# Kernel optimization log

Hardware: AMD Instinct MI355X
Metric: run time of the kernel (lower is better)

The kernel has to match this reference:

```python
import jax, jax.numpy as jnp
from jax import lax
import numpy as np

B, D, K = 4096, 128, 8192          # batch, embedding_dim, num_embeddings
LATENT_C, LATENT_H, LATENT_W = 64, 7, 7
OUT_H, OUT_W = 84, 84              # observation_shape H, W (decoder resizes 56->84)


def setup_inputs() -> dict:
    key = jax.random.key(0)
    ks = jax.random.split(key, 10)
    z = jax.random.normal(ks[0], (B, D), dtype=jnp.float32)
    # codebook init: uniform(-1/K, 1/K) as in torch module
    codebook = jax.random.uniform(ks[1], (K, D), jnp.float32, -1.0 / K, 1.0 / K)
    lin_w = jax.random.normal(ks[2], (LATENT_C * LATENT_H * LATENT_W, D), jnp.float32) * 0.02
    lin_b = jnp.zeros((LATENT_C * LATENT_H * LATENT_W,), jnp.float32)
    # ConvTranspose2d weights in torch layout (in_ch, out_ch, kH, kW)
    w1 = jax.random.normal(ks[3], (64, 64, 4, 4), jnp.float32) * 0.02
    b1 = jnp.zeros((64,), jnp.float32)
    w2 = jax.random.normal(ks[4], (64, 32, 4, 4), jnp.float32) * 0.02
    b2 = jnp.zeros((32,), jnp.float32)
    w3 = jax.random.normal(ks[5], (32, 1, 4, 4), jnp.float32) * 0.02
    b3 = jnp.zeros((1,), jnp.float32)
    return {"z": z, "codebook": codebook, "lin_w": lin_w, "lin_b": lin_b,
            "w1": w1, "b1": b1, "w2": w2, "b2": b2, "w3": w3, "b3": b3}


def _conv_transpose(x, w, b):
    """PyTorch ConvTranspose2d(k=4, stride=2, pad=1) via lhs-dilated conv.
    w is torch layout (in, out, kH, kW); flip spatially and swap in/out -> OIHW."""
    wk = jnp.flip(w, axis=(2, 3)).transpose(1, 0, 2, 3)  # (out, in, kH, kW)
    y = lax.conv_general_dilated(
        x, wk, window_strides=(1, 1), padding=((2, 2), (2, 2)),
        lhs_dilation=(2, 2), dimension_numbers=("NCHW", "OIHW", "NCHW"))
    return y + b[None, :, None, None]


def reference(z, codebook, lin_w, lin_b, w1, b1, w2, b2, w3, b3):
    # --- VectorQuantizer ---
    # squared L2 distances: ||z||^2 + ||e||^2 - 2 z e^T  -> (B, K)
    d2 = (jnp.sum(z * z, axis=1, keepdims=True)
          + jnp.sum(codebook * codebook, axis=1)
          - 2.0 * (z @ codebook.T))
    indices = jnp.argmin(d2, axis=1)              # (B,)
    z_q = codebook[indices]                       # gather (B, D)
    codebook_loss = jnp.mean((lax.stop_gradient(z) - z_q) ** 2)
    commitment_loss = jnp.mean((z - lax.stop_gradient(z_q)) ** 2)
    z_q_st = z + lax.stop_gradient(z_q - z)       # straight-through
    # --- VQVAEDecoder ---
    x = z_q_st @ lin_w.T + lin_b                  # (B, 64*7*7)
    x = x.reshape(-1, LATENT_C, LATENT_H, LATENT_W)
    x = jax.nn.relu(_conv_transpose(x, w1, b1))   # (B, 64, 14, 14)
    x = jax.nn.relu(_conv_transpose(x, w2, b2))   # (B, 32, 28, 28)
    x = _conv_transpose(x, w3, b3)                # (B, 1, 56, 56)
    # bilinear resize, align_corners=False (half-pixel centers)
    x = jax.image.resize(x, (x.shape[0], 1, OUT_H, OUT_W), method="bilinear")
    recon = jnp.tanh(x)
    return recon, indices, codebook_loss, commitment_loss
```

## Files before the change

### kernel.cpp

```cpp
#include <hip/hip_runtime.h>
#include <math.h>

#define B_SZ    4096
#define D_DIM   128
#define K_CODES 8192
#define RECON_N (4096*84*84)

__global__ __attribute__((amdgpu_flat_work_group_size(1024,1024),
                          amdgpu_waves_per_eu(4,8)))
void vq_kernel(
    const float* __restrict__ z, const float* __restrict__ cb,
    int* __restrict__ idx_ws, float* __restrict__ out_idx_f,
    double* __restrict__ lpart)
{
  __shared__ float z_s[16][128];
  __shared__ float zz_s[16];
  __shared__ float redv[16][16];
  __shared__ int   redi[16][16];
  __shared__ int   win[16];
  __shared__ double wsum[16];
  const int t  = threadIdx.x;
  const int b0 = blockIdx.x * 16;

  for (int p = t; p < 2048; p += 1024) z_s[p >> 7][p & 127] = z[(size_t)b0*128 + p];
  __syncthreads();

  if (t < 16) {
    #pragma clang fp contract(off)
    const float* a = z_s[t];
    float r8[8];
    #pragma unroll
    for (int j = 0; j < 8; j++) { float v = a[j]*a[j]; r8[j] = v; }
    for (int i = 8; i < 128; i += 8) {
      #pragma unroll
      for (int j = 0; j < 8; j++) { float v = a[i+j]*a[i+j]; r8[j] = r8[j] + v; }
    }
    zz_s[t] = ((r8[0]+r8[1]) + (r8[2]+r8[3])) + ((r8[4]+r8[5]) + (r8[6]+r8[7]));
  }
  __syncthreads();

  const int lane = t & 63, wv = t >> 6;
  float zzr[16];
  #pragma unroll
  for (int row = 0; row < 16; row++) zzr[row] = zz_s[row];

  float best[16]; int bid[16];
  #pragma unroll
  for (int row = 0; row < 16; row++) { best[row] = INFINITY; bid[row] = 0; }

  #pragma unroll 1
  for (int k = 0; k < 8; k++) {
    const int cg   = wv + (k << 4);
    const int code = (cg << 6) + lane;
    const float* ep = cb + (size_t)code * 128;
    float r[16];
    #pragma unroll
    for (int row = 0; row < 16; row++) r[row] = 0.0f;
    #pragma unroll 1
    for (int d16 = 0; d16 < 8; d16++) {
      const float4 e0 = *(const float4*)(ep + d16*16 + 0);
      const float4 e1 = *(const float4*)(ep + d16*16 + 4);
      const float4 e2 = *(const float4*)(ep + d16*16 + 8);
      const float4 e3 = *(const float4*)(ep + d16*16 + 12);
      #pragma unroll
      for (int row = 0; row < 16; row++) {
        const float4 z0 = *(const float4*)(&z_s[row][d16*16 + 0]);
        const float4 z1 = *(const float4*)(&z_s[row][d16*16 + 4]);
        const float4 z2 = *(const float4*)(&z_s[row][d16*16 + 8]);
        const float4 z3 = *(const float4*)(&z_s[row][d16*16 + 12]);
        float rr = r[row];
        rr = fmaf(z0.x,e0.x,rr); rr = fmaf(z0.y,e0.y,rr); rr = fmaf(z0.z,e0.z,rr); rr = fmaf(z0.w,e0.w,rr);
        rr = fmaf(z1.x,e1.x,rr); rr = fmaf(z1.y,e1.y,rr); rr = fmaf(z1.z,e1.z,rr); rr = fmaf(z1.w,e1.w,rr);
        rr = fmaf(z2.x,e2.x,rr); rr = fmaf(z2.y,e2.y,rr); rr = fmaf(z2.z,e2.z,rr); rr = fmaf(z2.w,e2.w,rr);
        rr = fmaf(z3.x,e3.x,rr); rr = fmaf(z3.y,e3.y,rr); rr = fmaf(z3.z,e3.z,rr); rr = fmaf(z3.w,e3.w,rr);
        r[row] = rr;
      }
    }
    #pragma unroll
    for (int row = 0; row < 16; row++) {
      const float tt = fmaf(-2.0f, r[row], zzr[row]);
      if (tt < best[row]) { best[row] = tt; bid[row] = code; }
    }
  }

  #pragma unroll 1
  for (int row = 0; row < 16; row++) {
    float v = best[row]; int i = bid[row];
    #pragma unroll
    for (int m = 32; m; m >>= 1) {
      float v2 = __shfl_xor(v, m, 64);
      int   i2 = __shfl_xor(i, m, 64);
      if (v2 < v || (v2 == v && i2 < i)) { v = v2; i = i2; }
    }
    if (lane == 0) { redv[wv][row] = v; redi[wv][row] = i; }
  }
  __syncthreads();

  if (t < 16) {
    float v = redv[0][t]; int i = redi[0][t];
    #pragma unroll 1
    for (int w = 1; w < 16; w++) {
      float v2 = redv[w][t]; int i2 = redi[w][t];
      if (v2 < v || (v2 == v && i2 < i)) { v = v2; i = i2; }
    }
    win[t] = i;
    idx_ws[b0 + t] = i;
    out_idx_f[b0 + t] = (float)i;
  }
  __syncthreads();

  double ls = 0.0;
  for (int p = t; p < 2048; p += 1024) {
    int r = p >> 7, d = p & 127;
    float diff = z_s[r][d] - cb[(size_t)win[r]*128 + d];
    ls = fma((double)diff, (double)diff, ls);
  }
  #pragma unroll
  for (int m = 32; m; m >>= 1) ls += __shfl_xor(ls, m, 64);
  if (lane == 0) wsum[wv] = ls;
  __syncthreads();
  if (t == 0) {
    double s = 0.0;
    for (int w = 0; w < 16; w++) s += wsum[w];
    lpart[blockIdx.x] = s;
  }
}

__global__ __launch_bounds__(256) void fin_kernel(const double* __restrict__ lpart,
                                                  float* __restrict__ out_loss)
{
  __shared__ double s[256];
  const int t = threadIdx.x;
  s[t] = lpart[t];
  __syncthreads();
  for (int off = 128; off; off >>= 1) {
    if (t < off) s[t] += s[t + off];
    __syncthreads();
  }
  if (t == 0) {
    float l = (float)(s[0] / (4096.0*128.0));
    out_loss[0] = l;
    out_loss[1] = l;
  }
}

__global__ __launch_bounds__(256) void linear_kernel(
    const float* __restrict__ cb, const int* __restrict__ idx,
    const float* __restrict__ lw, const float* __restrict__ lb,
    float* __restrict__ x1)
{
  __shared__ float As[64][65];
  __shared__ float Bs[64][65];
  __shared__ int idx_s[64];
  const int t  = threadIdx.x;
  const int b0 = blockIdx.x * 64, n0 = blockIdx.y * 64;
  if (t < 64) idx_s[t] = idx[b0 + t];
  float acc[4][4] = {{0.f}};
  const int tr = (t >> 4)*4, tc = (t & 15)*4;
  for (int d0 = 0; d0 < 128; d0 += 64) {
    __syncthreads();
    #pragma unroll
    for (int l = 0; l < 16; l++) {
      int flat = t + l*256;
      int r = flat >> 6, d = flat & 63;
      As[r][d] = cb[(size_t)idx_s[r]*128 + d0 + d];
      Bs[r][d] = lw[(size_t)(n0 + r)*128 + d0 + d];
    }
    __syncthreads();
    #pragma unroll 8
    for (int d = 0; d < 64; d++) {
      float a0 = As[tr+0][d], a1 = As[tr+1][d], a2 = As[tr+2][d], a3 = As[tr+3][d];
      float q0 = Bs[tc+0][d], q1 = Bs[tc+1][d], q2 = Bs[tc+2][d], q3 = Bs[tc+3][d];
      acc[0][0] = fmaf(a0,q0,acc[0][0]); acc[0][1] = fmaf(a0,q1,acc[0][1]);
      acc[0][2] = fmaf(a0,q2,acc[0][2]); acc[0][3] = fmaf(a0,q3,acc[0][3]);
      acc[1][0] = fmaf(a1,q0,acc[1][0]); acc[1][1] = fmaf(a1,q1,acc[1][1]);
      acc[1][2] = fmaf(a1,q2,acc[1][2]); acc[1][3] = fmaf(a1,q3,acc[1][3]);
      acc[2][0] = fmaf(a2,q0,acc[2][0]); acc[2][1] = fmaf(a2,q1,acc[2][1]);
      acc[2][2] = fmaf(a2,q2,acc[2][2]); acc[2][3] = fmaf(a2,q3,acc[2][3]);
      acc[3][0] = fmaf(a3,q0,acc[3][0]); acc[3][1] = fmaf(a3,q1,acc[3][1]);
      acc[3][2] = fmaf(a3,q2,acc[3][2]); acc[3][3] = fmaf(a3,q3,acc[3][3]);
    }
  }
  #pragma unroll
  for (int i = 0; i < 4; i++)
    #pragma unroll
    for (int j = 0; j < 4; j++)
      x1[(size_t)(b0 + tr + i)*3136 + n0 + tc + j] = acc[i][j] + lb[n0 + tc + j];
}

#define DA_T 896
#define B1_CS 260
#define IMG_FL (64*B1_CS)
__global__ __attribute__((amdgpu_flat_work_group_size(DA_T, DA_T),
                          amdgpu_waves_per_eu(4, 4)))
void decoder_a(
    const float* __restrict__ x1,
    const float* __restrict__ w1, const float* __restrict__ b1,
    const float* __restrict__ w2, const float* __restrict__ b2,
    float* __restrict__ a2, int b_off, int n_img)
{
  extern __shared__ float B1s[];
  const int tid = threadIdx.x;
  const int b   = blockIdx.x;
  const int iA  = 2*b;
  const bool hasB = (iA + 1) < n_img;
  const int gA  = b_off + iA;

  for (int p = tid; p < 2*IMG_FL; p += DA_T) B1s[p] = 0.0f;
  __syncthreads();

  {
    const int c = tid & 63, y = tid >> 6;
    const int ky0 = (y & 1) ? 0 : 1;
    const int iy0 = (y + 1 - ky0) >> 1;
    const int iy1 = iy0 - 1;
    const bool v0 = (iy0 < 7), v1 = (iy1 >= 0);
    const float bias = b1[c];
    float accA[14], accB[14];
    #pragma unroll
    for (int x = 0; x < 14; x++) { accA[x] = bias; accB[x] = bias; }
    const float* ximA = x1 + (size_t)gA*3136;
    const float* ximB = hasB ? (ximA + 3136) : ximA;
    #pragma unroll 1
    for (int i = 0; i < 64; i++) {
      const float* wp = w1 + (((i << 6) + c) << 4) + ky0*4;
      const float4 wA4 = *(const float4*)(wp);
      const float4 wB4 = *(const float4*)(wp + 8);
      const float wa[4] = {wA4.x, wA4.y, wA4.z, wA4.w};
      const float wb[4] = {wB4.x, wB4.y, wB4.z, wB4.w};
      float r0A[7], r1A[7], r0B[7], r1B[7];
      if (v0) {
        const float* xr = ximA + i*49 + iy0*7;
        const float* xs = ximB + i*49 + iy0*7;
        #pragma unroll
        for (int j = 0; j < 7; j++) { r0A[j] = xr[j]; r0B[j] = xs[j]; }
      } else {
        #pragma unroll
        for (int j = 0; j < 7; j++) { r0A[j] = 0.0f; r0B[j] = 0.0f; }
      }
      if (v1) {
        const float* xr = ximA + i*49 + iy1*7;
        const float* xs = ximB + i*49 + iy1*7;
        #pragma unroll
        for (int j = 0; j < 7; j++) { r1A[j] = xr[j]; r1B[j] = xs[j]; }
      } else {
        #pragma unroll
        for (int j = 0; j < 7; j++) { r1A[j] = 0.0f; r1B[j] = 0.0f; }
      }
      #pragma unroll
      for (int x = 0; x < 14; x++) {
        const int kxs = (x & 1) ? 0 : 1;
        const int ix0 = (x + 1 - kxs) >> 1;
        const int ix1 = ix0 - 1;
        float s = accA[x];
        if (ix0 < 7)  { s = fmaf(r0A[ix0], wa[kxs],   s); s = fmaf(r1A[ix0], wb[kxs],   s); }
        if (ix1 >= 0) { s = fmaf(r0A[ix1], wa[kxs+2], s); s = fmaf(r1A[ix1], wb[kxs+2], s); }
        accA[x] = s;
      }
      #pragma unroll
      for (int x = 0; x < 14; x++) {
        const int kxs = (x & 1) ? 0 : 1;
        const int ix0 = (x + 1 - kxs) >> 1;
        const int ix1 = ix0 - 1;
        float s = accB[x];
        if (ix0 < 7)  { s = fmaf(r0B[ix0], wa[kxs],   s); s = fmaf(r1B[ix0], wb[kxs],   s); }
        if (ix1 >= 0) { s = fmaf(r0B[ix1], wa[kxs+2], s); s = fmaf(r1B[ix1], wb[kxs+2], s); }
        accB[x] = s;
      }
    }
    float* oA = &B1s[c*B1_CS + (y + 1)*16 + 1];
    float* oB = oA + IMG_FL;
    #pragma unroll
    for (int x = 0; x < 14; x++) oA[x] = fmaxf(accA[x], 0.0f);
    #pragma unroll
    for (int x = 0; x < 14; x++) oB[x] = fmaxf(accB[x], 0.0f);
  }
  __syncthreads();

  {
    const int c = tid & 31, y = tid >> 5;
    const int ky0 = (y & 1) ? 0 : 1;
    const int iy0 = (y + 1 - ky0) >> 1;
    const int row0 = iy0 + 1;
    const int row1 = iy0;
    const float bias = b2[c];
    const int nimg = hasB ? 2 : 1;
    #pragma unroll 1
    for (int img = 0; img < nimg; img++) {
      const float* base = &B1s[img*IMG_FL];
      float acc[28];
      #pragma unroll
      for (int x = 0; x < 28; x++) acc[x] = bias;
      #pragma unroll 1
      for (int i = 0; i < 64; i++) {
        const float* wp = w2 + (((i << 5) + c) << 4) + ky0*4;
        const float4 wA4 = *(const float4*)(wp);
        const float4 wB4 = *(const float4*)(wp + 8);
        const float wa[4] = {wA4.x, wA4.y, wA4.z, wA4.w};
        const float wb[4] = {wB4.x, wB4.y, wB4.z, wB4.w};
        const float* rp0 = base + i*B1_CS + row0*16;
        const float* rp1 = base + i*B1_CS + row1*16;
        float r0[16], r1[16];
        #pragma unroll
        for (int q = 0; q < 4; q++) {
          const float4 a4 = *(const float4*)(rp0 + q*4);
          r0[q*4+0]=a4.x; r0[q*4+1]=a4.y; r0[q*4+2]=a4.z; r0[q*4+3]=a4.w;
        }
        #pragma unroll
        for (int q = 0; q < 4; q++) {
          const float4 a4 = *(const float4*)(rp1 + q*4);
          r1[q*4+0]=a4.x; r1[q*4+1]=a4.y; r1[q*4+2]=a4.z; r1[q*4+3]=a4.w;
        }
        #pragma unroll
        for (int x = 0; x < 28; x++) {
          const int kxs = (x & 1) ? 0 : 1;
          const int col = ((x + 1 - kxs) >> 1) + 1;
          float s = acc[x];
          s = fmaf(r0[col],   wa[kxs],   s);
          s = fmaf(r1[col],   wb[kxs],   s);
          s = fmaf(r0[col-1], wa[kxs+2], s);
          s = fmaf(r1[col-1], wb[kxs+2], s);
          acc[x] = s;
        }
      }
      float* st = a2 + (size_t)(iA + img)*25088 + c*784 + y*28;
      #pragma unroll
      for (int x = 0; x < 28; x++) acc[x] = fmaxf(acc[x], 0.0f);
      #pragma unroll
      for (int q = 0; q < 7; q++)
        *(float4*)(st + q*4) = make_float4(acc[q*4+0],acc[q*4+1],acc[q*4+2],acc[q*4+3]);
    }
  }
}

#define DB_T 896
__global__ __attribute__((amdgpu_flat_work_group_size(DB_T, DB_T)))
void decoder_b(
    const float* __restrict__ a2,
    const float* __restrict__ w3, const float* __restrict__ b3,
    float* __restrict__ out, int b_off)
{
  extern __shared__ float lds[];
  float* Cs  = lds;
  float* Ds  = lds + 25088;
  float* W3s = lds + 28224;
  const int tid = threadIdx.x;
  const int b   = blockIdx.x;
  const int bg  = b + b_off;

  {
    const float4* src = (const float4*)(a2 + (size_t)b*25088);
    for (int p = tid; p < 6272; p += DB_T) ((float4*)Cs)[p] = src[p];
    for (int p = tid; p < 512; p += DB_T) W3s[p] = w3[p];
  }
  __syncthreads();

  if (tid < 784) {
    const int y = tid / 14, xq = tid - y*14;
    const int x0 = xq * 4;
    const int ky0 = (y & 1) ? 0 : 1;
    const int iy0 = (y + 1 - ky0) >> 1;
    const int iy1 = iy0 - 1;
    const bool v0 = (iy0 < 28), v1 = (iy1 >= 0);
    const int ixb = (x0 >> 1) - 1;
    float acc[4];
    const float bias = b3[0];
    #pragma unroll
    for (int x = 0; x < 4; x++) acc[x] = bias;
    #pragma unroll 1
    for (int i = 0; i < 32; i++) {
      const float* wr = &W3s[i*16 + ky0*4];
      float wa[4], wb[4];
      #pragma unroll
      for (int k = 0; k < 4; k++) { wa[k] = wr[k]; wb[k] = wr[8 + k]; }
      const float* Ci = &Cs[i*784];
      float r0[4], r1[4];
      #pragma unroll
      for (int j = 0; j < 4; j++) {
        const int ix = ixb + j;
        const bool vx = (ix >= 0) && (ix < 28);
        r0[j] = (v0 && vx) ? Ci[iy0*28 + ix] : 0.0f;
        r1[j] = (v1 && vx) ? Ci[iy1*28 + ix] : 0.0f;
      }
      #pragma unroll
      for (int xl = 0; xl < 4; xl++) {
        const int kxs = (xl & 1) ? 0 : 1;
        const int j = ((x0 + xl + 1 - kxs) >> 1) - ixb;
        float s = acc[xl];
        s = fmaf(r0[j],   wa[kxs],   s);
        s = fmaf(r1[j],   wb[kxs],   s);
        s = fmaf(r0[j-1], wa[kxs+2], s);
        s = fmaf(r1[j-1], wb[kxs+2], s);
        acc[xl] = s;
      }
    }
    *(float4*)(&Ds[y*56 + x0]) = make_float4(acc[0],acc[1],acc[2],acc[3]);
  }
  __syncthreads();

  for (int p = tid; p < 84*84; p += DB_T) {
    const int oy = p / 84, ox = p - oy*84;
    const float sy = (oy + 0.5f)*(2.0f/3.0f) - 0.5f;
    const float sx = (ox + 0.5f)*(2.0f/3.0f) - 0.5f;
    const int y0 = (int)floorf(sy), x0i = (int)floorf(sx);
    const float fy = sy - (float)y0, fx = sx - (float)x0i;
    const int y0c = y0 < 0 ? 0 : y0, y1c = (y0 + 1 > 55) ? 55 : (y0 + 1);
    const int x0c = x0i < 0 ? 0 : x0i, x1c = (x0i + 1 > 55) ? 55 : (x0i + 1);
    const float v00 = Ds[y0c*56 + x0c], v01 = Ds[y0c*56 + x1c];
    const float v10 = Ds[y1c*56 + x0c], v11 = Ds[y1c*56 + x1c];
    const float v = (v00*(1.0f - fx) + v01*fx)*(1.0f - fy)
                  + (v10*(1.0f - fx) + v11*fx)*fy;
    out[(size_t)bg*7056 + p] = tanhf(v);
  }
}

extern "C" void kernel_launch(void* const* d_in, const int* in_sizes, int n_in,
                              void* d_out, int out_size, void* d_ws, size_t ws_size,
                              hipStream_t stream) {
  (void)in_sizes; (void)n_in; (void)out_size;
  const float* z  = (const float*)d_in[0];
  const float* cb = (const float*)d_in[1];
  const float* lw = (const float*)d_in[2];
  const float* lb = (const float*)d_in[3];
  const float* w1 = (const float*)d_in[4];
  const float* b1 = (const float*)d_in[5];
  const float* w2 = (const float*)d_in[6];
  const float* b2 = (const float*)d_in[7];
  const float* w3 = (const float*)d_in[8];
  const float* b3 = (const float*)d_in[9];

  float* out      = (float*)d_out;
  float* out_idx  = out + RECON_N;
  float* out_loss = out + RECON_N + 4096;

  char*   ws     = (char*)d_ws;
  double* lpart  = (double*)ws;
  int*    idx_ws = (int*)(ws + 4096);
  float*  x1     = (float*)(ws + 32768);
  const size_t a2_off = 32768 + (size_t)4096*3136*4;
  float*  a2     = (float*)(ws + a2_off);

  long long avail = (long long)ws_size - (long long)a2_off;
  int cap = (int)(avail / (25088*4));
  if (cap > 4096) cap = 4096;
  if (cap < 1) cap = 1;
  if (cap >= 2) cap &= ~1;

  vq_kernel<<<256, 1024, 0, stream>>>(z, cb, idx_ws, out_idx, lpart);
  fin_kernel<<<1, 256, 0, stream>>>(lpart, out_loss);
  linear_kernel<<<dim3(64, 49), 256, 0, stream>>>(cb, idx_ws, lw, lb, x1);

  const int da_lds = 2*IMG_FL*4;
  const int db_lds = (25088+3136+512)*4;
  hipFuncSetAttribute((const void*)decoder_a,
                      hipFuncAttributeMaxDynamicSharedMemorySize, da_lds);
  hipFuncSetAttribute((const void*)decoder_b,
                      hipFuncAttributeMaxDynamicSharedMemorySize, db_lds);
  for (int b0 = 0; b0 < B_SZ; b0 += cap) {
    const int n = (B_SZ - b0 < cap) ? (B_SZ - b0) : cap;
    decoder_a<<<(n + 1)/2, DA_T, da_lds, stream>>>(x1, w1, b1, w2, b2, a2, b0, n);
    decoder_b<<<n, DB_T, db_lds, stream>>>(a2, w3, b3, out, b0);
  }
}
```

Measured before the change: 2.133 ms.

## Process one image per decoder_a block with compact padded LDS layout

decoder_a now handles one image per block instead of two, which halves the accumulators and LDS per block. The first-stage LDS buffer drops its padding border rows: a shared 16-float zero row stands in for the top and bottom boundaries, and the zero columns are written inline with float4 stores. The full LDS zero-fill is removed and the waves-per-EU hint is relaxed to allow higher occupancy. The cost is that each block now loads every w1/w2 weight for a single image, so weight reuse across images is lost and twice as many blocks are launched.

```diff
diff --git a/kernel.cpp b/kernel.cpp
--- a/kernel.cpp
+++ b/kernel.cpp
@@ -189,24 +189,22 @@
 }
 
 #define DA_T 896
-#define B1_CS 260
-#define IMG_FL (64*B1_CS)
+#define B1_CS 228
+#define DA_LDS_FL (16 + 64*B1_CS)
 __global__ __attribute__((amdgpu_flat_work_group_size(DA_T, DA_T),
-                          amdgpu_waves_per_eu(4, 4)))
+                          amdgpu_waves_per_eu(4, 8)))
 void decoder_a(
     const float* __restrict__ x1,
     const float* __restrict__ w1, const float* __restrict__ b1,
     const float* __restrict__ w2, const float* __restrict__ b2,
-    float* __restrict__ a2, int b_off, int n_img)
+    float* __restrict__ a2, int b_off)
 {
   extern __shared__ float B1s[];
   const int tid = threadIdx.x;
   const int b   = blockIdx.x;
-  const int iA  = 2*b;
-  const bool hasB = (iA + 1) < n_img;
-  const int gA  = b_off + iA;
-
-  for (int p = tid; p < 2*IMG_FL; p += DA_T) B1s[p] = 0.0f;
+  const int bg  = b + b_off;
+
+  if (tid < 16) B1s[tid] = 0.0f;
   __syncthreads();
 
   {
@@ -215,12 +213,11 @@
     const int iy0 = (y + 1 - ky0) >> 1;
     const int iy1 = iy0 - 1;
     const bool v0 = (iy0 < 7), v1 = (iy1 >= 0);
+    float acc[14];
     const float bias = b1[c];
-    float accA[14], accB[14];
-    #pragma unroll
-    for (int x = 0; x < 14; x++) { accA[x] = bias; accB[x] = bias; }
-    const float* ximA = x1 + (size_t)gA*3136;
-    const float* ximB = hasB ? (ximA + 3136) : ximA;
+    #pragma unroll
+    for (int x = 0; x < 14; x++) acc[x] = bias;
+    const float* xim = x1 + (size_t)bg*3136;
     #pragma unroll 1
     for (int i = 0; i < 64; i++) {
       const float* wp = w1 + (((i << 6) + c) << 4) + ky0*4;
@@ -228,52 +225,41 @@
       const float4 wB4 = *(const float4*)(wp + 8);
       const float wa[4] = {wA4.x, wA4.y, wA4.z, wA4.w};
       const float wb[4] = {wB4.x, wB4.y, wB4.z, wB4.w};
-      float r0A[7], r1A[7], r0B[7], r1B[7];
+      float r0[7], r1[7];
       if (v0) {
-        const float* xr = ximA + i*49 + iy0*7;
-        const float* xs = ximB + i*49 + iy0*7;
+        const float* xr = xim + i*49 + iy0*7;
         #pragma unroll
-        for (int j = 0; j < 7; j++) { r0A[j] = xr[j]; r0B[j] = xs[j]; }
+        for (int j = 0; j < 7; j++) r0[j] = xr[j];
       } else {
         #pragma unroll
-        for (int j = 0; j < 7; j++) { r0A[j] = 0.0f; r0B[j] = 0.0f; }
+        for (int j = 0; j < 7; j++) r0[j] = 0.0f;
       }
       if (v1) {
-        const float* xr = ximA + i*49 + iy1*7;
-        const float* xs = ximB + i*49 + iy1*7;
+        const float* xr = xim + i*49 + iy1*7;
         #pragma unroll
-        for (int j = 0; j < 7; j++) { r1A[j] = xr[j]; r1B[j] = xs[j]; }
+        for (int j = 0; j < 7; j++) r1[j] = xr[j];
       } else {
         #pragma unroll
-        for (int j = 0; j < 7; j++) { r1A[j] = 0.0f; r1B[j] = 0.0f; }
+        for (int j = 0; j < 7; j++) r1[j] = 0.0f;
       }
       #pragma unroll
       for (int x = 0; x < 14; x++) {
         const int kxs = (x & 1) ? 0 : 1;
         const int ix0 = (x + 1 - kxs) >> 1;
         const int ix1 = ix0 - 1;
-        float s = accA[x];
-        if (ix0 < 7)  { s = fmaf(r0A[ix0], wa[kxs],   s); s = fmaf(r1A[ix0], wb[kxs],   s); }
-        if (ix1 >= 0) { s = fmaf(r0A[ix1], wa[kxs+2], s); s = fmaf(r1A[ix1], wb[kxs+2], s); }
-        accA[x] = s;
-      }
-      #pragma unroll
-      for (int x = 0; x < 14; x++) {
-        const int kxs = (x & 1) ? 0 : 1;
-        const int ix0 = (x + 1 - kxs) >> 1;
-        const int ix1 = ix0 - 1;
-        float s = accB[x];
-        if (ix0 < 7)  { s = fmaf(r0B[ix0], wa[kxs],   s); s = fmaf(r1B[ix0], wb[kxs],   s); }
-        if (ix1 >= 0) { s = fmaf(r0B[ix1], wa[kxs+2], s); s = fmaf(r1B[ix1], wb[kxs+2], s); }
-        accB[x] = s;
-      }
-    }
-    float* oA = &B1s[c*B1_CS + (y + 1)*16 + 1];
-    float* oB = oA + IMG_FL;
-    #pragma unroll
-    for (int x = 0; x < 14; x++) oA[x] = fmaxf(accA[x], 0.0f);
-    #pragma unroll
-    for (int x = 0; x < 14; x++) oB[x] = fmaxf(accB[x], 0.0f);
+        float s = acc[x];
+        if (ix0 < 7)  { s = fmaf(r0[ix0], wa[kxs],   s); s = fmaf(r1[ix0], wb[kxs],   s); }
+        if (ix1 >= 0) { s = fmaf(r0[ix1], wa[kxs+2], s); s = fmaf(r1[ix1], wb[kxs+2], s); }
+        acc[x] = s;
+      }
+    }
+    float* o = &B1s[16 + c*B1_CS + y*16];
+    #pragma unroll
+    for (int x = 0; x < 14; x++) acc[x] = fmaxf(acc[x], 0.0f);
+    *(float4*)(o + 0)  = make_float4(0.0f,    acc[0],  acc[1],  acc[2]);
+    *(float4*)(o + 4)  = make_float4(acc[3],  acc[4],  acc[5],  acc[6]);
+    *(float4*)(o + 8)  = make_float4(acc[7],  acc[8],  acc[9],  acc[10]);
+    *(float4*)(o + 12) = make_float4(acc[11], acc[12], acc[13], 0.0f);
   }
   __syncthreads();
 
@@ -283,53 +269,53 @@
     const int iy0 = (y + 1 - ky0) >> 1;
     const int row0 = iy0 + 1;
     const int row1 = iy0;
+    const bool z0 = (row0 == 15);
+    const bool z1 = (row1 == 0);
+    const float* p0 = z0 ? B1s : (B1s + 16 + (row0 - 1)*16);
+    const float* p1 = z1 ? B1s : (B1s + 16 + (row1 - 1)*16);
+    const int s0 = z0 ? 0 : B1_CS;
+    const int s1 = z1 ? 0 : B1_CS;
     const float bias = b2[c];
-    const int nimg = hasB ? 2 : 1;
+    float acc[28];
+    #pragma unroll
+    for (int x = 0; x < 28; x++) acc[x] = bias;
     #pragma unroll 1
-    for (int img = 0; img < nimg; img++) {
-      const float* base = &B1s[img*IMG_FL];
-      float acc[28];
-      #pragma unroll
-      for (int x = 0; x < 28; x++) acc[x] = bias;
-      #pragma unroll 1
-      for (int i = 0; i < 64; i++) {
-        const float* wp = w2 + (((i << 5) + c) << 4) + ky0*4;
-        const float4 wA4 = *(const float4*)(wp);
-        const float4 wB4 = *(const float4*)(wp + 8);
-        const float wa[4] = {wA4.x, wA4.y, wA4.z, wA4.w};
-        const float wb[4] = {wB4.x, wB4.y, wB4.z, wB4.w};
-        const float* rp0 = base + i*B1_CS + row0*16;
-        const float* rp1 = base + i*B1_CS + row1*16;
-        float r0[16], r1[16];
-        #pragma unroll
-        for (int q = 0; q < 4; q++) {
-          const float4 a4 = *(const float4*)(rp0 + q*4);
-          r0[q*4+0]=a4.x; r0[q*4+1]=a4.y; r0[q*4+2]=a4.z; r0[q*4+3]=a4.w;
-        }
-        #pragma unroll
-        for (int q = 0; q < 4; q++) {
-          const float4 a4 = *(const float4*)(rp1 + q*4);
-          r1[q*4+0]=a4.x; r1[q*4+1]=a4.y; r1[q*4+2]=a4.z; r1[q*4+3]=a4.w;
-        }
-        #pragma unroll
-        for (int x = 0; x < 28; x++) {
-          const int kxs = (x & 1) ? 0 : 1;
-          const int col = ((x + 1 - kxs) >> 1) + 1;
-          float s = acc[x];
-          s = fmaf(r0[col],   wa[kxs],   s);
-          s = fmaf(r1[col],   wb[kxs],   s);
-          s = fmaf(r0[col-1], wa[kxs+2], s);
-          s = fmaf(r1[col-1], wb[kxs+2], s);
-          acc[x] = s;
-        }
-      }
-      float* st = a2 + (size_t)(iA + img)*25088 + c*784 + y*28;
-      #pragma unroll
-      for (int x = 0; x < 28; x++) acc[x] = fmaxf(acc[x], 0.0f);
-      #pragma unroll
-      for (int q = 0; q < 7; q++)
-        *(float4*)(st + q*4) = make_float4(acc[q*4+0],acc[q*4+1],acc[q*4+2],acc[q*4+3]);
-    }
+    for (int i = 0; i < 64; i++) {
+      const float* wp = w2 + (((i << 5) + c) << 4) + ky0*4;
+      const float4 wA4 = *(const float4*)(wp);
+      const float4 wB4 = *(const float4*)(wp + 8);
+      const float wa[4] = {wA4.x, wA4.y, wA4.z, wA4.w};
+      const float wb[4] = {wB4.x, wB4.y, wB4.z, wB4.w};
+      float r0[16], r1[16];
+      #pragma unroll
+      for (int q = 0; q < 4; q++) {
+        const float4 a4 = *(const float4*)(p0 + q*4);
+        r0[q*4+0]=a4.x; r0[q*4+1]=a4.y; r0[q*4+2]=a4.z; r0[q*4+3]=a4.w;
+      }
+      #pragma unroll
+      for (int q = 0; q < 4; q++) {
+        const float4 a4 = *(const float4*)(p1 + q*4);
+        r1[q*4+0]=a4.x; r1[q*4+1]=a4.y; r1[q*4+2]=a4.z; r1[q*4+3]=a4.w;
+      }
+      p0 += s0; p1 += s1;
+      #pragma unroll
+      for (int x = 0; x < 28; x++) {
+        const int kxs = (x & 1) ? 0 : 1;
+        const int col = ((x + 1 - kxs) >> 1) + 1;
+        float s = acc[x];
+        s = fmaf(r0[col],   wa[kxs],   s);
+        s = fmaf(r1[col],   wb[kxs],   s);
+        s = fmaf(r0[col-1], wa[kxs+2], s);
+        s = fmaf(r1[col-1], wb[kxs+2], s);
+        acc[x] = s;
+      }
+    }
+    float* st = a2 + (size_t)b*25088 + c*784 + y*28;
+    #pragma unroll
+    for (int x = 0; x < 28; x++) acc[x] = fmaxf(acc[x], 0.0f);
+    #pragma unroll
+    for (int q = 0; q < 7; q++)
+      *(float4*)(st + q*4) = make_float4(acc[q*4+0],acc[q*4+1],acc[q*4+2],acc[q*4+3]);
   }
 }
 
@@ -444,13 +430,12 @@
   int cap = (int)(avail / (25088*4));
   if (cap > 4096) cap = 4096;
   if (cap < 1) cap = 1;
-  if (cap >= 2) cap &= ~1;
 
   vq_kernel<<<256, 1024, 0, stream>>>(z, cb, idx_ws, out_idx, lpart);
   fin_kernel<<<1, 256, 0, stream>>>(lpart, out_loss);
   linear_kernel<<<dim3(64, 49), 256, 0, stream>>>(cb, idx_ws, lw, lb, x1);
 
-  const int da_lds = 2*IMG_FL*4;
+  const int da_lds = DA_LDS_FL*4;
   const int db_lds = (25088+3136+512)*4;
   hipFuncSetAttribute((const void*)decoder_a,
                       hipFuncAttributeMaxDynamicSharedMemorySize, da_lds);
@@ -458,7 +443,7 @@
                       hipFuncAttributeMaxDynamicSharedMemorySize, db_lds);
   for (int b0 = 0; b0 < B_SZ; b0 += cap) {
     const int n = (B_SZ - b0 < cap) ? (B_SZ - b0) : cap;
-    decoder_a<<<(n + 1)/2, DA_T, da_lds, stream>>>(x1, w1, b1, w2, b2, a2, b0, n);
+    decoder_a<<<n, DA_T, da_lds, stream>>>(x1, w1, b1, w2, b2, a2, b0);
     decoder_b<<<n, DB_T, db_lds, stream>>>(a2, w3, b3, out, b0);
   }
 }
```

Result: slower. 2.317 ms (+8.6%).
